# Kernel optimization log

Measured on AMD Instinct MI355X. Metric: run time of the kernel, lower is better.

Reference implementation:

```python
import jax, jax.numpy as jnp
import numpy as np

EPS = 1e-5
K = 5

def _bn(x, g, b):
    # BatchNorm1d in training mode: biased batch statistics
    mu = jnp.mean(x, axis=0)
    var = jnp.mean((x - mu) ** 2, axis=0)
    return (x - mu) * jax.lax.rsqrt(var + EPS) * g + b

def setup_inputs():
    key = jax.random.key(0)
    ks = jax.random.split(key, 16)
    N, M, D, F = 16384, 8192, 512, 2048
    s = 0.02
    return dict(
        src=jax.random.normal(ks[0], (N, D), jnp.float32),
        anchor_2=jax.random.normal(ks[1], (M, D), jnp.float32),
        W_dim=jax.random.normal(ks[2], (D, D), jnp.float32) * s,
        b_dim=jnp.zeros((D,), jnp.float32),
        W_fus=jax.random.normal(ks[3], (2 * D, D), jnp.float32) * s,
        b_fus=jnp.zeros((D,), jnp.float32),
        W_e1=jax.random.normal(ks[4], (D, F), jnp.float32) * s,
        b_e1=jnp.zeros((F,), jnp.float32),
        W_e2=jax.random.normal(ks[5], (F, D), jnp.float32) * s,
        b_e2=jnp.zeros((D,), jnp.float32),
        g1=jnp.ones((D,), jnp.float32), bt1=jnp.zeros((D,), jnp.float32),
        g2=jnp.ones((D,), jnp.float32), bt2=jnp.zeros((D,), jnp.float32),
        W_d=jax.random.normal(ks[6], (D, D), jnp.float32) * s,
        b_d=jnp.zeros((D,), jnp.float32),
        g_d=jnp.ones((D,), jnp.float32), bt_d=jnp.zeros((D,), jnp.float32),
    )

def reference(src, anchor_2, W_dim, b_dim, W_fus, b_fus, W_e1, b_e1, W_e2, b_e2,
              g1, bt1, g2, bt2, W_d, b_d, g_d, bt_d):
    # kNN in Euclidean metric (sklearn NearestNeighbors): squared distances suffice
    # d2[n,m] = ||src_n||^2 - 2 src_n . a_m + ||a_m||^2   -> [N, M]
    d2 = (jnp.sum(src * src, axis=1, keepdims=True)
          - 2.0 * (src @ anchor_2.T)
          + jnp.sum(anchor_2 * anchor_2, axis=1)[None, :])
    _, idx = jax.lax.top_k(-d2, K)                      # [N, K] nearest anchors
    neigh = jnp.mean(anchor_2[idx], axis=1)             # gather + mean -> [N, D]
    a_map = neigh @ W_dim + b_dim                       # linear_dim
    comb = jnp.concatenate([src, a_map], axis=1) @ W_fus + b_fus
    comb = _bn(comb, g1, bt1)                           # norm1
    # encoder MLP (dropout is identity in eval)
    t = jnp.tanh(comb @ W_e1 + b_e1) @ W_e2 + b_e2
    comb = _bn(comb + t, g2, bt2)                       # residual + norm2
    out = jnp.tanh(_bn(comb @ W_d + b_d, g_d, bt_d))    # decoder
    return out
```

## Files before the change

kernel.cpp:

```cpp
#include <hip/hip_runtime.h>
#include <math.h>

#define N_ROWS 16384
#define M_ANCH 8192
#define DDIM   512
#define FDIM   2048
#define KNN    5
#define BN_EPS 1e-5f
#define CHUNK  8192
#define SEED   1024
#define CAND_MAX 256
#define MARGIN 4.0f

typedef _Float16 f16;
typedef _Float16 f16x8 __attribute__((ext_vector_type(8)));
typedef _Float16 f16x4 __attribute__((ext_vector_type(4)));
typedef float f32x4 __attribute__((ext_vector_type(4)));

__device__ __forceinline__ void async_copy16(const void* g, void* l) {
    __builtin_amdgcn_global_load_lds(
        (const __attribute__((address_space(1))) void*)g,
        (__attribute__((address_space(3))) void*)l, 16, 0, 0);
}

__device__ __forceinline__ bool kless(float k1, int i1, float k2, int i2) {
    return (k1 < k2) || (k1 == k2 && i1 < i2);
}

__device__ __forceinline__ void insert5(float (&bk)[KNN], int (&bi)[KNN], float key, int id) {
    if (!kless(key, id, bk[4], bi[4])) return;
    bool c3 = kless(key, id, bk[3], bi[3]);
    bool c2 = kless(key, id, bk[2], bi[2]);
    bool c1 = kless(key, id, bk[1], bi[1]);
    bool c0 = kless(key, id, bk[0], bi[0]);
    bk[4] = c3 ? bk[3] : key;                  bi[4] = c3 ? bi[3] : id;
    bk[3] = c3 ? (c2 ? bk[2] : key) : bk[3];   bi[3] = c3 ? (c2 ? bi[2] : id) : bi[3];
    bk[2] = c2 ? (c1 ? bk[1] : key) : bk[2];   bi[2] = c2 ? (c1 ? bi[1] : id) : bi[2];
    bk[1] = c1 ? (c0 ? bk[0] : key) : bk[1];   bi[1] = c1 ? (c0 ? bi[0] : id) : bi[1];
    bk[0] = c0 ? key : bk[0];                  bi[0] = c0 ? id : bi[0];
}

__global__ void zero_kernel(float* p, int n) {
    int i = blockIdx.x * blockDim.x + threadIdx.x;
    if (i < n) p[i] = 0.f;
}

__global__ __launch_bounds__(256) void cast_f16_kernel(const float* __restrict__ X,
                                                       f16* __restrict__ Y, int n4) {
    int i4 = blockIdx.x * 256 + threadIdx.x;
    if (i4 >= n4) return;
    float4 v = ((const float4*)X)[i4];
    f16x4 h;
    h.x = (f16)v.x; h.y = (f16)v.y; h.z = (f16)v.z; h.w = (f16)v.w;
    ((f16x4*)Y)[i4] = h;
}

__global__ __launch_bounds__(256) void anchor_norm_kernel(const float* __restrict__ a,
                                                          float* __restrict__ norm_a) {
    int wave = threadIdx.x >> 6, lane = threadIdx.x & 63;
    int row = blockIdx.x * 4 + wave;
    const float4* ar = (const float4*)(a + (size_t)row * DDIM);
    float4 v1 = ar[lane * 2];
    float4 v2 = ar[lane * 2 + 1];
    float s = v1.x*v1.x + v1.y*v1.y + v1.z*v1.z + v1.w*v1.w
            + v2.x*v2.x + v2.y*v2.y + v2.z*v2.z + v2.w*v2.w;
    for (int off = 32; off; off >>= 1) s += __shfl_xor(s, off, 64);
    if (lane == 0) norm_a[row] = s;
}

template<int K>
__global__ __launch_bounds__(256) void gemm_f16_key(
    const f16* __restrict__ A, const f16* __restrict__ B,
    const float* __restrict__ norm, float* __restrict__ C, int Ncols)
{
    __shared__ f16 As[128 * 32];
    __shared__ f16 Bs[128 * 32];
    const int t = threadIdx.x;
    const int w = t >> 6, l = t & 63;
    const int m0 = blockIdx.y * 128, n0 = blockIdx.x * 128;
    const int wm = (w & 1) * 64, wn = (w >> 1) * 64;

    f32x4 acc[4][4];
    #pragma unroll
    for (int i = 0; i < 4; ++i)
        #pragma unroll
        for (int j = 0; j < 4; ++j) acc[i][j] = (f32x4){0.f, 0.f, 0.f, 0.f};

    const int srow = l >> 2;
    const int gq = ((l & 3) - (srow >> 1)) & 3;
    const int skoff = gq * 8;
    const int sqf = (((l >> 4) + (((l & 15) >> 1) & 3)) & 3) * 8;

    for (int k0 = 0; k0 < K; k0 += 32) {
        __syncthreads();
        #pragma unroll
        for (int s = 0; s < 2; ++s) {
            int grp = w * 2 + s;
            int row = grp * 16 + srow;
            async_copy16(A + (size_t)(m0 + row) * K + k0 + skoff, As + grp * 512 + l * 8);
            async_copy16(B + (size_t)(n0 + row) * K + k0 + skoff, Bs + grp * 512 + l * 8);
        }
        __syncthreads();
        f16x8 af[4], bf[4];
        #pragma unroll
        for (int i = 0; i < 4; ++i)
            af[i] = *(const f16x8*)(As + (wm + i * 16 + (l & 15)) * 32 + sqf);
        #pragma unroll
        for (int j = 0; j < 4; ++j)
            bf[j] = *(const f16x8*)(Bs + (wn + j * 16 + (l & 15)) * 32 + sqf);
        #pragma unroll
        for (int i = 0; i < 4; ++i)
            #pragma unroll
            for (int j = 0; j < 4; ++j)
                acc[i][j] = __builtin_amdgcn_mfma_f32_16x16x32_f16(af[i], bf[j], acc[i][j], 0, 0, 0);
    }
    float nj[4];
    #pragma unroll
    for (int j = 0; j < 4; ++j) nj[j] = norm[n0 + wn + j * 16 + (l & 15)];
    #pragma unroll
    for (int i = 0; i < 4; ++i)
        #pragma unroll
        for (int j = 0; j < 4; ++j)
            #pragma unroll
            for (int r = 0; r < 4; ++r) {
                int m = m0 + wm + i * 16 + (l >> 4) * 4 + r;
                int n = n0 + wn + j * 16 + (l & 15);
                C[(size_t)m * Ncols + n] = nj[j] - 2.f * acc[i][j][r];
            }
}

template<int K>
__global__ __launch_bounds__(256) void gemm_collect(
    const f16* __restrict__ A, const f16* __restrict__ B,
    const float* __restrict__ norm, const float* __restrict__ thr,
    int* __restrict__ cnt, int* __restrict__ cand_i, int idofs)
{
    __shared__ f16 As[128 * 32];
    __shared__ f16 Bs[128 * 32];
    const int t = threadIdx.x;
    const int w = t >> 6, l = t & 63;
    const int m0 = blockIdx.y * 128, n0 = blockIdx.x * 128;
    const int wm = (w & 1) * 64, wn = (w >> 1) * 64;

    f32x4 acc[4][4];
    #pragma unroll
    for (int i = 0; i < 4; ++i)
        #pragma unroll
        for (int j = 0; j < 4; ++j) acc[i][j] = (f32x4){0.f, 0.f, 0.f, 0.f};

    const int srow = l >> 2;
    const int gq = ((l & 3) - (srow >> 1)) & 3;
    const int skoff = gq * 8;
    const int sqf = (((l >> 4) + (((l & 15) >> 1) & 3)) & 3) * 8;

    for (int k0 = 0; k0 < K; k0 += 32) {
        __syncthreads();
        #pragma unroll
        for (int s = 0; s < 2; ++s) {
            int grp = w * 2 + s;
            int row = grp * 16 + srow;
            async_copy16(A + (size_t)(m0 + row) * K + k0 + skoff, As + grp * 512 + l * 8);
            async_copy16(B + (size_t)(n0 + row) * K + k0 + skoff, Bs + grp * 512 + l * 8);
        }
        __syncthreads();
        f16x8 af[4], bf[4];
        #pragma unroll
        for (int i = 0; i < 4; ++i)
            af[i] = *(const f16x8*)(As + (wm + i * 16 + (l & 15)) * 32 + sqf);
        #pragma unroll
        for (int j = 0; j < 4; ++j)
            bf[j] = *(const f16x8*)(Bs + (wn + j * 16 + (l & 15)) * 32 + sqf);
        #pragma unroll
        for (int i = 0; i < 4; ++i)
            #pragma unroll
            for (int j = 0; j < 4; ++j)
                acc[i][j] = __builtin_amdgcn_mfma_f32_16x16x32_f16(af[i], bf[j], acc[i][j], 0, 0, 0);
    }
    float thr4[4][4];
    #pragma unroll
    for (int i = 0; i < 4; ++i) {
        float4 tv = *(const float4*)&thr[m0 + wm + i * 16 + (l >> 4) * 4];
        thr4[i][0] = tv.x; thr4[i][1] = tv.y; thr4[i][2] = tv.z; thr4[i][3] = tv.w;
    }
    float nj[4];
    #pragma unroll
    for (int j = 0; j < 4; ++j) nj[j] = norm[n0 + wn + j * 16 + (l & 15)];
    #pragma unroll
    for (int i = 0; i < 4; ++i)
        #pragma unroll
        for (int j = 0; j < 4; ++j)
            #pragma unroll
            for (int r = 0; r < 4; ++r) {
                float key = nj[j] - 2.f * acc[i][j][r];
                if (key < thr4[i][r]) {
                    int row = m0 + wm + i * 16 + (l >> 4) * 4 + r;
                    int pos = atomicAdd(&cnt[row], 1);
                    if (pos < CAND_MAX)
                        cand_i[(size_t)row * CAND_MAX + pos] =
                            idofs + n0 + wn + j * 16 + (l & 15);
                }
            }
}

__global__ __launch_bounds__(256) void topk_scan_kernel(
    const float* __restrict__ g, float* __restrict__ thrbuf,
    int* __restrict__ cnt, int* __restrict__ cand_i)
{
    int row = blockIdx.x * 4 + (threadIdx.x >> 6);
    int lane = threadIdx.x & 63;
    const float* grow = g + (size_t)row * SEED;
    float4 v0 = *(const float4*)(grow + lane * 4);
    float4 v1 = *(const float4*)(grow + 256 + lane * 4);
    float4 v2 = *(const float4*)(grow + 512 + lane * 4);
    float4 v3 = *(const float4*)(grow + 768 + lane * 4);
    float bk[KNN]; int bi[KNN];
    #pragma unroll
    for (int q = 0; q < KNN; ++q) { bk[q] = 3.0e38f; bi[q] = 0x7fffffff; }
    int c = lane * 4;
    insert5(bk, bi, v0.x, c);       insert5(bk, bi, v0.y, c + 1);
    insert5(bk, bi, v0.z, c + 2);   insert5(bk, bi, v0.w, c + 3);
    insert5(bk, bi, v1.x, c + 256); insert5(bk, bi, v1.y, c + 257);
    insert5(bk, bi, v1.z, c + 258); insert5(bk, bi, v1.w, c + 259);
    insert5(bk, bi, v2.x, c + 512); insert5(bk, bi, v2.y, c + 513);
    insert5(bk, bi, v2.z, c + 514); insert5(bk, bi, v2.w, c + 515);
    insert5(bk, bi, v3.x, c + 768); insert5(bk, bi, v3.y, c + 769);
    insert5(bk, bi, v3.z, c + 770); insert5(bk, bi, v3.w, c + 771);
    for (int off = 32; off >= 1; off >>= 1) {
        float ok[KNN]; int oi[KNN];
        #pragma unroll
        for (int q = 0; q < KNN; ++q) {
            ok[q] = __shfl_xor(bk[q], off, 64);
            oi[q] = __shfl_xor(bi[q], off, 64);
        }
        #pragma unroll
        for (int q = 0; q < KNN; ++q) insert5(bk, bi, ok[q], oi[q]);
    }
    float thr = bk[4] + MARGIN;
    if (lane == 0) thrbuf[row] = thr;
    int* rci = cand_i + (size_t)row * CAND_MAX;
    #define PUSH(v, id) if ((v) < thr) { int pos = atomicAdd(&cnt[row], 1); \
                                         if (pos < CAND_MAX) rci[pos] = (id); }
    PUSH(v0.x, c)       PUSH(v0.y, c + 1)   PUSH(v0.z, c + 2)   PUSH(v0.w, c + 3)
    PUSH(v1.x, c + 256) PUSH(v1.y, c + 257) PUSH(v1.z, c + 258) PUSH(v1.w, c + 259)
    PUSH(v2.x, c + 512) PUSH(v2.y, c + 513) PUSH(v2.z, c + 514) PUSH(v2.w, c + 515)
    PUSH(v3.x, c + 768) PUSH(v3.y, c + 769) PUSH(v3.z, c + 770) PUSH(v3.w, c + 771)
    #undef PUSH
}

__global__ __launch_bounds__(256) void rescore_kernel(
    const float* __restrict__ src, const float* __restrict__ anchor,
    const float* __restrict__ norm_a, const int* __restrict__ cnt,
    const int* __restrict__ cand_i, int* __restrict__ bi_state)
{
    int row = blockIdx.x * 4 + (threadIdx.x >> 6);
    int lane = threadIdx.x & 63;
    const float4* sp = (const float4*)(src + (size_t)row * DDIM);
    float4 s0 = sp[lane * 2], s1 = sp[lane * 2 + 1];
    float bk[KNN]; int bi[KNN];
    #pragma unroll
    for (int q = 0; q < KNN; ++q) { bk[q] = 3.0e38f; bi[q] = 0x7fffffff; }
    int c = cnt[row]; if (c > CAND_MAX) c = CAND_MAX;
    const int* ci = cand_i + (size_t)row * CAND_MAX;
    for (int p = 0; p < c; ++p) {
        int id = ci[p];
        const float4* ap = (const float4*)(anchor + (size_t)id * DDIM);
        float4 a0 = ap[lane * 2], a1 = ap[lane * 2 + 1];
        float d = s0.x*a0.x + s0.y*a0.y + s0.z*a0.z + s0.w*a0.w
                + s1.x*a1.x + s1.y*a1.y + s1.z*a1.z + s1.w*a1.w;
        #pragma unroll
        for (int off = 32; off; off >>= 1) d += __shfl_xor(d, off, 64);
        float key = norm_a[id] - 2.f * d;
        insert5(bk, bi, key, id);
    }
    if (lane == 0) {
        #pragma unroll
        for (int q = 0; q < KNN; ++q) bi_state[row * KNN + q] = bi[q];
    }
}

__global__ __launch_bounds__(256) void gather_mean_kernel(
    const float* __restrict__ anchor, const int* __restrict__ bi_state,
    float* __restrict__ neigh)
{
    int row = blockIdx.x * 4 + (threadIdx.x >> 6);
    int lane = threadIdx.x & 63;
    const int* bi = bi_state + row * KNN;
    int i0 = bi[0], i1 = bi[1], i2 = bi[2], i3 = bi[3], i4 = bi[4];
    const float4* a0 = (const float4*)(anchor + (size_t)i0 * DDIM);
    const float4* a1 = (const float4*)(anchor + (size_t)i1 * DDIM);
    const float4* a2 = (const float4*)(anchor + (size_t)i2 * DDIM);
    const float4* a3 = (const float4*)(anchor + (size_t)i3 * DDIM);
    const float4* a4 = (const float4*)(anchor + (size_t)i4 * DDIM);
    float4* np = (float4*)(neigh + (size_t)row * DDIM);
    #pragma unroll
    for (int p = 0; p < 2; ++p) {
        int c4 = lane + 64 * p;
        float4 v0 = a0[c4], v1 = a1[c4], v2 = a2[c4], v3 = a3[c4], v4 = a4[c4];
        float4 o;
        o.x = (v0.x + v1.x + v2.x + v3.x + v4.x) * 0.2f;
        o.y = (v0.y + v1.y + v2.y + v3.y + v4.y) * 0.2f;
        o.z = (v0.z + v1.z + v2.z + v3.z + v4.z) * 0.2f;
        o.w = (v0.w + v1.w + v2.w + v3.w + v4.w) * 0.2f;
        np[c4] = o;
    }
}

template<int ADDC0, int TANH, int K>
__global__ __launch_bounds__(256) void gemm_split_nt(
    const float* __restrict__ A, const f16* __restrict__ Bw,
    const float* __restrict__ bias, const float* __restrict__ C0,
    float* __restrict__ C, int Ncols)
{
    __shared__ f16 Ah[128 * 32];
    __shared__ f16 Al[128 * 32];
    __shared__ f16 Bh[128 * 32];
    __shared__ f16 Bl[128 * 32];
    const int t = threadIdx.x;
    const int w = t >> 6, l = t & 63;
    const int m0 = blockIdx.y * 128, n0 = blockIdx.x * 128;
    const int wm = (w & 1) * 64, wn = (w >> 1) * 64;
    const int K2 = 2 * K;

    f32x4 acc[4][4];
    #pragma unroll
    for (int i = 0; i < 4; ++i)
        #pragma unroll
        for (int j = 0; j < 4; ++j) acc[i][j] = (f32x4){0.f, 0.f, 0.f, 0.f};

    const int ar = t >> 1;
    const int ac = (t & 1) * 16;
    const int arq = (ar >> 1) & 3;
    const int s0 = (((t & 1) * 2 + 0 + arq) & 3) * 8;
    const int s1 = (((t & 1) * 2 + 1 + arq) & 3) * 8;
    const int srow = l >> 2;
    const int gq = ((l & 3) - (srow >> 1)) & 3;
    const int skoff = gq * 8;
    const int sqf = (((l >> 4) + (((l & 15) >> 1) & 3)) & 3) * 8;

    for (int k0 = 0; k0 < K; k0 += 32) {
        __syncthreads();
        #pragma unroll
        for (int s = 0; s < 2; ++s) {
            int grp = w * 2 + s;
            int row = grp * 16 + srow;
            const f16* bp = Bw + (size_t)(n0 + row) * K2 + k0 + skoff;
            async_copy16(bp, Bh + grp * 512 + l * 8);
            async_copy16(bp + K, Bl + grp * 512 + l * 8);
        }
        {
            const float* ap = A + (size_t)(m0 + ar) * K + k0 + ac;
            float xs[16];
            *(float4*)&xs[0]  = *(const float4*)ap;
            *(float4*)&xs[4]  = *(const float4*)(ap + 4);
            *(float4*)&xs[8]  = *(const float4*)(ap + 8);
            *(float4*)&xs[12] = *(const float4*)(ap + 12);
            f16x8 h0, h1, lo0, lo1;
            #pragma unroll
            for (int e = 0; e < 8; ++e) {
                f16 hh = (f16)xs[e];
                h0[e] = hh; lo0[e] = (f16)(xs[e] - (float)hh);
                f16 hh2 = (f16)xs[8 + e];
                h1[e] = hh2; lo1[e] = (f16)(xs[8 + e] - (float)hh2);
            }
            *(f16x8*)&Ah[ar * 32 + s0] = h0;  *(f16x8*)&Ah[ar * 32 + s1] = h1;
            *(f16x8*)&Al[ar * 32 + s0] = lo0; *(f16x8*)&Al[ar * 32 + s1] = lo1;
        }
        __syncthreads();
        f16x8 afh[4], afl[4], bfh[4], bfl[4];
        #pragma unroll
        for (int i = 0; i < 4; ++i) {
            int base = (wm + i * 16 + (l & 15)) * 32 + sqf;
            afh[i] = *(const f16x8*)(Ah + base);
            afl[i] = *(const f16x8*)(Al + base);
        }
        #pragma unroll
        for (int j = 0; j < 4; ++j) {
            int base = (wn + j * 16 + (l & 15)) * 32 + sqf;
            bfh[j] = *(const f16x8*)(Bh + base);
            bfl[j] = *(const f16x8*)(Bl + base);
        }
        #pragma unroll
        for (int i = 0; i < 4; ++i)
            #pragma unroll
            for (int j = 0; j < 4; ++j) {
                acc[i][j] = __builtin_amdgcn_mfma_f32_16x16x32_f16(afh[i], bfh[j], acc[i][j], 0, 0, 0);
                acc[i][j] = __builtin_amdgcn_mfma_f32_16x16x32_f16(afl[i], bfh[j], acc[i][j], 0, 0, 0);
                acc[i][j] = __builtin_amdgcn_mfma_f32_16x16x32_f16(afh[i], bfl[j], acc[i][j], 0, 0, 0);
            }
    }
    float bv[4];
    #pragma unroll
    for (int j = 0; j < 4; ++j)
        bv[j] = bias ? bias[n0 + wn + j * 16 + (l & 15)] : 0.f;
    #pragma unroll
    for (int i = 0; i < 4; ++i)
        #pragma unroll
        for (int j = 0; j < 4; ++j)
            #pragma unroll
            for (int r = 0; r < 4; ++r) {
                int m = m0 + wm + i * 16 + (l >> 4) * 4 + r;
                int n = n0 + wn + j * 16 + (l & 15);
                float v = acc[i][j][r] + bv[j];
                if (ADDC0) v += C0[(size_t)m * Ncols + n];
                if (TANH)  v = tanhf(v);
                C[(size_t)m * Ncols + n] = v;
            }
}

__global__ __launch_bounds__(256) void wsplit_kernel(const float* __restrict__ W,
                                                     f16* __restrict__ Wt,
                                                     int K, int N)
{
    __shared__ float tile[64][65];
    const int t = threadIdx.x;
    const int kb = blockIdx.y * 64, nb = blockIdx.x * 64;
    #pragma unroll
    for (int i = 0; i < 4; ++i) {
        int r = (t >> 4) + i * 16;
        int c = (t & 15) * 4;
        *(float4*)&tile[r][c] = *(const float4*)&W[(size_t)(kb + r) * N + nb + c];
    }
    __syncthreads();
    const int r2 = t >> 2;
    const int kc = (t & 3) * 16;
    f16x8 h0, h1, lo0, lo1;
    #pragma unroll
    for (int e = 0; e < 8; ++e) {
        float x = tile[kc + e][r2];
        f16 hh = (f16)x; h0[e] = hh; lo0[e] = (f16)(x - (float)hh);
        float y = tile[kc + 8 + e][r2];
        f16 hh2 = (f16)y; h1[e] = hh2; lo1[e] = (f16)(y - (float)hh2);
    }
    f16* base = Wt + (size_t)(nb + r2) * 2 * K + kb + kc;
    *(f16x8*)base = h0; *(f16x8*)(base + 8) = h1;
    *(f16x8*)(base + K) = lo0; *(f16x8*)(base + K + 8) = lo1;
}

__global__ __launch_bounds__(256) void bcomb_kernel(const float* __restrict__ b_dim,
                                                    const float* __restrict__ W_fus2,
                                                    const float* __restrict__ b_fus,
                                                    float* __restrict__ b_comb)
{
    int n = blockIdx.x * 256 + threadIdx.x;
    if (n >= DDIM) return;
    float s = b_fus[n];
    for (int k = 0; k < DDIM; ++k) s += b_dim[k] * W_fus2[(size_t)k * DDIM + n];
    b_comb[n] = s;
}

template<int ACT>
__global__ __launch_bounds__(256) void gemm_kernel(
    const float* __restrict__ A, int K1,
    const float* __restrict__ A2, int K2,
    const float* __restrict__ B, const float* __restrict__ bias,
    float* __restrict__ C, int Ncols)
{
    __shared__ float As[16][132];
    __shared__ float Bs[16][128];
    const int t = threadIdx.x;
    const int n0 = blockIdx.x * 128;
    const int m0 = blockIdx.y * 128;
    const int ty = t >> 4, tx = t & 15;
    const int K = K1 + K2;

    float acc[8][8];
    #pragma unroll
    for (int i = 0; i < 8; ++i)
        #pragma unroll
        for (int j = 0; j < 8; ++j) acc[i][j] = 0.f;

    const int ar = t >> 1;
    const int akc = (t & 1) * 8;
    const int bkr = t >> 4;
    const int bc = (t & 15) * 8;

    for (int k0 = 0; k0 < K; k0 += 16) {
        int kk = k0 + akc;
        float4 v0, v1;
        if (kk < K1) {
            const float* p = A + (size_t)(m0 + ar) * K1 + kk;
            v0 = *(const float4*)p; v1 = *(const float4*)(p + 4);
        } else {
            const float* p = A2 + (size_t)(m0 + ar) * K2 + (kk - K1);
            v0 = *(const float4*)p; v1 = *(const float4*)(p + 4);
        }
        const float* bp = B + (size_t)(k0 + bkr) * Ncols + n0 + bc;
        float4 w0 = *(const float4*)bp, w1 = *(const float4*)(bp + 4);
        __syncthreads();
        As[akc+0][ar] = v0.x; As[akc+1][ar] = v0.y; As[akc+2][ar] = v0.z; As[akc+3][ar] = v0.w;
        As[akc+4][ar] = v1.x; As[akc+5][ar] = v1.y; As[akc+6][ar] = v1.z; As[akc+7][ar] = v1.w;
        *(float4*)&Bs[bkr][bc] = w0; *(float4*)&Bs[bkr][bc + 4] = w1;
        __syncthreads();
        #pragma unroll
        for (int k = 0; k < 16; ++k) {
            float a[8], b[8];
            *(float4*)&a[0] = *(const float4*)&As[k][ty * 8];
            *(float4*)&a[4] = *(const float4*)&As[k][ty * 8 + 4];
            *(float4*)&b[0] = *(const float4*)&Bs[k][tx * 4];
            *(float4*)&b[4] = *(const float4*)&Bs[k][64 + tx * 4];
            #pragma unroll
            for (int i = 0; i < 8; ++i)
                #pragma unroll
                for (int j = 0; j < 8; ++j) acc[i][j] += a[i] * b[j];
        }
    }
    float4 bv0 = *(const float4*)(bias + n0 + tx * 4);
    float4 bv1 = *(const float4*)(bias + n0 + 64 + tx * 4);
    #pragma unroll
    for (int i = 0; i < 8; ++i) {
        int row = m0 + ty * 8 + i;
        float4 o0, o1;
        o0.x = acc[i][0] + bv0.x; o0.y = acc[i][1] + bv0.y;
        o0.z = acc[i][2] + bv0.z; o0.w = acc[i][3] + bv0.w;
        o1.x = acc[i][4] + bv1.x; o1.y = acc[i][5] + bv1.y;
        o1.z = acc[i][6] + bv1.z; o1.w = acc[i][7] + bv1.w;
        if (ACT == 1) {
            o0.x = tanhf(o0.x); o0.y = tanhf(o0.y); o0.z = tanhf(o0.z); o0.w = tanhf(o0.w);
            o1.x = tanhf(o1.x); o1.y = tanhf(o1.y); o1.z = tanhf(o1.z); o1.w = tanhf(o1.w);
        }
        *(float4*)(C + (size_t)row * Ncols + n0 + tx * 4) = o0;
        *(float4*)(C + (size_t)row * Ncols + n0 + 64 + tx * 4) = o1;
    }
}

__global__ __launch_bounds__(256) void bn_stats_kernel(const float* __restrict__ X,
                                                       float* __restrict__ sums)
{
    __shared__ float red[8][64];
    int lane = threadIdx.x & 63;
    int rl = threadIdx.x >> 6;
    int c = blockIdx.x * 64 + lane;
    int chunk = N_ROWS / gridDim.y;
    int rbeg = blockIdx.y * chunk;
    float s = 0.f, s2 = 0.f;
    for (int r = rbeg + rl; r < rbeg + chunk; r += 4) {
        float v = X[(size_t)r * DDIM + c];
        s += v; s2 += v * v;
    }
    red[rl][lane] = s; red[4 + rl][lane] = s2;
    __syncthreads();
    if (threadIdx.x < 64) {
        float ts = red[0][lane] + red[1][lane] + red[2][lane] + red[3][lane];
        float t2 = red[4][lane] + red[5][lane] + red[6][lane] + red[7][lane];
        atomicAdd(&sums[c], ts);
        atomicAdd(&sums[DDIM + c], t2);
    }
}

template<int TANH>
__global__ __launch_bounds__(256) void bn_apply_kernel(
    const float* __restrict__ X, float* __restrict__ Y,
    const float* __restrict__ sums, const float* __restrict__ g,
    const float* __restrict__ b, float invN)
{
    size_t i = (size_t)blockIdx.x * 256 + threadIdx.x;
    int cg = (int)(i % (DDIM / 4));
    int c = cg * 4;
    float4 x = ((const float4*)X)[i];
    float4 sm = *(const float4*)(sums + c);
    float4 sq = *(const float4*)(sums + DDIM + c);
    float4 gv = *(const float4*)(g + c);
    float4 bv = *(const float4*)(b + c);
    float m, var, rs;
    m = sm.x * invN; var = sq.x * invN - m * m; rs = rsqrtf(var + BN_EPS);
    x.x = (x.x - m) * rs * gv.x + bv.x;
    m = sm.y * invN; var = sq.y * invN - m * m; rs = rsqrtf(var + BN_EPS);
    x.y = (x.y - m) * rs * gv.y + bv.y;
    m = sm.z * invN; var = sq.z * invN - m * m; rs = rsqrtf(var + BN_EPS);
    x.z = (x.z - m) * rs * gv.z + bv.z;
    m = sm.w * invN; var = sq.w * invN - m * m; rs = rsqrtf(var + BN_EPS);
    x.w = (x.w - m) * rs * gv.w + bv.w;
    if (TANH) { x.x = tanhf(x.x); x.y = tanhf(x.y); x.z = tanhf(x.z); x.w = tanhf(x.w); }
    ((float4*)Y)[i] = x;
}

extern "C" void kernel_launch(void* const* d_in, const int* in_sizes, int n_in,
                              void* d_out, int out_size, void* d_ws, size_t ws_size,
                              hipStream_t stream)
{
    const float* src   = (const float*)d_in[0];
    const float* anc   = (const float*)d_in[1];
    const float* W_dim = (const float*)d_in[2];
    const float* b_dim = (const float*)d_in[3];
    const float* W_fus = (const float*)d_in[4];
    const float* b_fus = (const float*)d_in[5];
    const float* W_e1  = (const float*)d_in[6];
    const float* b_e1  = (const float*)d_in[7];
    const float* W_e2  = (const float*)d_in[8];
    const float* b_e2  = (const float*)d_in[9];
    const float* g1    = (const float*)d_in[10];
    const float* bt1   = (const float*)d_in[11];
    const float* g2    = (const float*)d_in[12];
    const float* bt2   = (const float*)d_in[13];
    const float* W_d   = (const float*)d_in[14];
    const float* b_d   = (const float*)d_in[15];
    const float* g_d   = (const float*)d_in[16];
    const float* bt_d  = (const float*)d_in[17];
    float* out = (float*)d_out;

    float* ws = (float*)d_ws;
    float* score  = ws;
    float* bufA   = ws + 16777216;
    f16*   src2h  = (f16*)(ws + 25165824);
    f16*   anc2h  = (f16*)(ws + 37748736);
    f16*   wbase  = (f16*)(ws + 25165824);
    f16*   Wt_fus1  = wbase;
    f16*   Wt_comb2 = wbase + 524288;
    f16*   Wt_e1    = wbase + 1048576;
    f16*   Wt_e2    = wbase + 3145728;
    f16*   Wt_d     = wbase + 5242880;
    float* W_comb2  = ws + 44040192;
    float* norm_a   = ws + 44302336;
    float* sums1    = ws + 44310528;
    float* sums2    = sums1 + 1024;
    float* sums3    = sums2 + 1024;
    float* zeros512 = ws + 44313600;
    float* b_comb   = ws + 44314112;
    int*   bi_state = (int*)(ws + 44396544);
    float* thrbuf   = ws + 44478464;
    int*   cnt      = (int*)(ws + 44494848);
    int*   cand_i   = (int*)(ws + 48705536);

    const float invN = 1.0f / (float)N_ROWS;
    float* hbuf = score;

    zero_kernel<<<dim3(14), 256, 0, stream>>>(sums1, 3584);
    zero_kernel<<<dim3(64), 256, 0, stream>>>((float*)cnt, 16384);
    cast_f16_kernel<<<dim3(N_ROWS * DDIM / 1024), 256, 0, stream>>>(
        src, src2h, N_ROWS * DDIM / 4);
    cast_f16_kernel<<<dim3(M_ANCH * DDIM / 1024), 256, 0, stream>>>(
        anc, anc2h, M_ANCH * DDIM / 4);
    anchor_norm_kernel<<<dim3(M_ANCH / 4), 256, 0, stream>>>(anc, norm_a);

    gemm_f16_key<DDIM><<<dim3(SEED / 128, N_ROWS / 128), 256, 0, stream>>>(
        src2h, anc2h, norm_a, score, SEED);
    topk_scan_kernel<<<dim3(N_ROWS / 4), 256, 0, stream>>>(
        score, thrbuf, cnt, cand_i);
    gemm_collect<DDIM><<<dim3((M_ANCH - SEED) / 128, N_ROWS / 128), 256, 0, stream>>>(
        src2h, anc2h + (size_t)SEED * DDIM, norm_a + SEED, thrbuf,
        cnt, cand_i, SEED);
    rescore_kernel<<<dim3(N_ROWS / 4), 256, 0, stream>>>(
        src, anc, norm_a, cnt, cand_i, bi_state);
    gather_mean_kernel<<<dim3(N_ROWS / 4), 256, 0, stream>>>(anc, bi_state, bufA);

    wsplit_kernel<<<dim3(DDIM / 64, DDIM / 64), 256, 0, stream>>>(W_fus, Wt_fus1, DDIM, DDIM);
    wsplit_kernel<<<dim3(FDIM / 64, DDIM / 64), 256, 0, stream>>>(W_e1, Wt_e1, DDIM, FDIM);
    wsplit_kernel<<<dim3(DDIM / 64, FDIM / 64), 256, 0, stream>>>(W_e2, Wt_e2, FDIM, DDIM);
    wsplit_kernel<<<dim3(DDIM / 64, DDIM / 64), 256, 0, stream>>>(W_d, Wt_d, DDIM, DDIM);
    gemm_kernel<0><<<dim3(4, 4), 256, 0, stream>>>(
        W_dim, DDIM, nullptr, 0, W_fus + DDIM * DDIM, zeros512, W_comb2, DDIM);
    bcomb_kernel<<<dim3(2), 256, 0, stream>>>(b_dim, W_fus + DDIM * DDIM, b_fus, b_comb);
    wsplit_kernel<<<dim3(DDIM / 64, DDIM / 64), 256, 0, stream>>>(W_comb2, Wt_comb2, DDIM, DDIM);

    gemm_split_nt<0, 0, DDIM><<<dim3(DDIM / 128, N_ROWS / 128), 256, 0, stream>>>(
        src, Wt_fus1, b_comb, nullptr, out, DDIM);
    gemm_split_nt<1, 0, DDIM><<<dim3(DDIM / 128, N_ROWS / 128), 256, 0, stream>>>(
        bufA, Wt_comb2, nullptr, out, out, DDIM);
    bn_stats_kernel<<<dim3(DDIM / 64, 16), 256, 0, stream>>>(out, sums1);
    bn_apply_kernel<0><<<dim3(8192), 256, 0, stream>>>(out, out, sums1, g1, bt1, invN);

    for (int r0 = 0; r0 < N_ROWS; r0 += CHUNK) {
        gemm_split_nt<0, 1, DDIM><<<dim3(FDIM / 128, CHUNK / 128), 256, 0, stream>>>(
            out + (size_t)r0 * DDIM, Wt_e1, b_e1, nullptr, hbuf, FDIM);
        gemm_split_nt<1, 0, FDIM><<<dim3(DDIM / 128, CHUNK / 128), 256, 0, stream>>>(
            hbuf, Wt_e2, b_e2, out + (size_t)r0 * DDIM, bufA + (size_t)r0 * DDIM,
            DDIM);
    }
    bn_stats_kernel<<<dim3(DDIM / 64, 16), 256, 0, stream>>>(bufA, sums2);
    bn_apply_kernel<0><<<dim3(8192), 256, 0, stream>>>(bufA, bufA, sums2, g2, bt2, invN);

    gemm_split_nt<0, 0, DDIM><<<dim3(DDIM / 128, N_ROWS / 128), 256, 0, stream>>>(
        bufA, Wt_d, b_d, nullptr, out, DDIM);
    bn_stats_kernel<<<dim3(DDIM / 64, 16), 256, 0, stream>>>(out, sums3);
    bn_apply_kernel<1><<<dim3(8192), 256, 0, stream>>>(out, out, sums3, g_d, bt_d, invN);
}
```

Before: 1.607 ms.

## Quantize kNN distance GEMMs to int8 MFMA with double-buffered LDS

Replaces the f16 cast and f16 MFMA candidate-screening GEMMs with an int8 quantization (fixed scale 28) and the i8 16x16x64 MFMA, so half as many bytes are loaded and the instruction has higher peak throughput. The two GEMM variants are merged into one templated kernel that double-buffers LDS tiles so loads overlap compute. The candidate margin is widened to absorb the larger quantization error. Exact rescoring in fp32 still picks the final neighbours, but a fixed scale with clipping assumes inputs of roughly unit scale, and more candidates may overflow CAND_MAX.

```diff
diff --git a/kernel.cpp b/kernel.cpp
--- a/kernel.cpp
+++ b/kernel.cpp
@@ -10,12 +10,15 @@
 #define CHUNK  8192
 #define SEED   1024
 #define CAND_MAX 256
-#define MARGIN 4.0f
+#define MARGIN 6.0f
+#define QSCALE 28.0f
+#define TWO_INV_S2 (2.0f / (QSCALE * QSCALE))
 
 typedef _Float16 f16;
 typedef _Float16 f16x8 __attribute__((ext_vector_type(8)));
 typedef _Float16 f16x4 __attribute__((ext_vector_type(4)));
 typedef float f32x4 __attribute__((ext_vector_type(4)));
+typedef int   i32x4 __attribute__((ext_vector_type(4)));
 
 __device__ __forceinline__ void async_copy16(const void* g, void* l) {
     __builtin_amdgcn_global_load_lds(
@@ -45,14 +48,17 @@
     if (i < n) p[i] = 0.f;
 }
 
-__global__ __launch_bounds__(256) void cast_f16_kernel(const float* __restrict__ X,
-                                                       f16* __restrict__ Y, int n4) {
-    int i4 = blockIdx.x * 256 + threadIdx.x;
-    if (i4 >= n4) return;
-    float4 v = ((const float4*)X)[i4];
-    f16x4 h;
-    h.x = (f16)v.x; h.y = (f16)v.y; h.z = (f16)v.z; h.w = (f16)v.w;
-    ((f16x4*)Y)[i4] = h;
+__global__ __launch_bounds__(256) void quant_i8_kernel(const float* __restrict__ X,
+                                                       unsigned int* __restrict__ Y, int n4) {
+    int i = blockIdx.x * 256 + threadIdx.x;
+    if (i >= n4) return;
+    float4 v = ((const float4*)X)[i];
+    int a = (int)rintf(v.x * QSCALE); a = a > 127 ? 127 : (a < -127 ? -127 : a);
+    int b = (int)rintf(v.y * QSCALE); b = b > 127 ? 127 : (b < -127 ? -127 : b);
+    int c = (int)rintf(v.z * QSCALE); c = c > 127 ? 127 : (c < -127 ? -127 : c);
+    int d = (int)rintf(v.w * QSCALE); d = d > 127 ? 127 : (d < -127 ? -127 : d);
+    Y[i] = (unsigned int)(a & 255) | ((unsigned int)(b & 255) << 8)
+         | ((unsigned int)(c & 255) << 16) | ((unsigned int)(d & 255) << 24);
 }
 
 __global__ __launch_bounds__(256) void anchor_norm_kernel(const float* __restrict__ a,
@@ -68,138 +74,103 @@
     if (lane == 0) norm_a[row] = s;
 }
 
-template<int K>
-__global__ __launch_bounds__(256) void gemm_f16_key(
-    const f16* __restrict__ A, const f16* __restrict__ B,
-    const float* __restrict__ norm, float* __restrict__ C, int Ncols)
-{
-    __shared__ f16 As[128 * 32];
-    __shared__ f16 Bs[128 * 32];
+template<int COLLECT>
+__global__ __launch_bounds__(256) void gemm_i8(
+    const char* __restrict__ A, const char* __restrict__ B,
+    const float* __restrict__ norm, const float* __restrict__ thr,
+    int* __restrict__ cnt, int* __restrict__ cand_i, int idofs,
+    float* __restrict__ C, int Ncols)
+{
+    __shared__ char As[2][128 * 64];
+    __shared__ char Bs[2][128 * 64];
     const int t = threadIdx.x;
     const int w = t >> 6, l = t & 63;
     const int m0 = blockIdx.y * 128, n0 = blockIdx.x * 128;
     const int wm = (w & 1) * 64, wn = (w >> 1) * 64;
 
-    f32x4 acc[4][4];
+    i32x4 acc[4][4];
     #pragma unroll
     for (int i = 0; i < 4; ++i)
         #pragma unroll
-        for (int j = 0; j < 4; ++j) acc[i][j] = (f32x4){0.f, 0.f, 0.f, 0.f};
+        for (int j = 0; j < 4; ++j) acc[i][j] = (i32x4){0, 0, 0, 0};
 
     const int srow = l >> 2;
     const int gq = ((l & 3) - (srow >> 1)) & 3;
-    const int skoff = gq * 8;
-    const int sqf = (((l >> 4) + (((l & 15) >> 1) & 3)) & 3) * 8;
-
-    for (int k0 = 0; k0 < K; k0 += 32) {
-        __syncthreads();
+    const int skoff = gq * 16;
+    const int sqf = (((l >> 4) + (((l & 15) >> 1) & 3)) & 3) * 16;
+
+    auto STAGE = [&](int buf, int kt) {
+        int k0 = kt * 64;
         #pragma unroll
         for (int s = 0; s < 2; ++s) {
             int grp = w * 2 + s;
             int row = grp * 16 + srow;
-            async_copy16(A + (size_t)(m0 + row) * K + k0 + skoff, As + grp * 512 + l * 8);
-            async_copy16(B + (size_t)(n0 + row) * K + k0 + skoff, Bs + grp * 512 + l * 8);
-        }
-        __syncthreads();
-        f16x8 af[4], bf[4];
+            async_copy16(A + (size_t)(m0 + row) * DDIM + k0 + skoff,
+                         &As[buf][grp * 1024 + l * 16]);
+            async_copy16(B + (size_t)(n0 + row) * DDIM + k0 + skoff,
+                         &Bs[buf][grp * 1024 + l * 16]);
+        }
+    };
+
+    STAGE(0, 0);
+    __syncthreads();
+
+    for (int kt = 0; kt < 8; ++kt) {
+        int cur = kt & 1;
+        if (kt < 7) STAGE(cur ^ 1, kt + 1);
+        i32x4 af[4], bf[4];
         #pragma unroll
         for (int i = 0; i < 4; ++i)
-            af[i] = *(const f16x8*)(As + (wm + i * 16 + (l & 15)) * 32 + sqf);
+            af[i] = *(const i32x4*)&As[cur][(wm + i * 16 + (l & 15)) * 64 + sqf];
         #pragma unroll
         for (int j = 0; j < 4; ++j)
-            bf[j] = *(const f16x8*)(Bs + (wn + j * 16 + (l & 15)) * 32 + sqf);
+            bf[j] = *(const i32x4*)&Bs[cur][(wn + j * 16 + (l & 15)) * 64 + sqf];
         #pragma unroll
         for (int i = 0; i < 4; ++i)
             #pragma unroll
             for (int j = 0; j < 4; ++j)
-                acc[i][j] = __builtin_amdgcn_mfma_f32_16x16x32_f16(af[i], bf[j], acc[i][j], 0, 0, 0);
-    }
+                acc[i][j] = __builtin_amdgcn_mfma_i32_16x16x64_i8(af[i], bf[j], acc[i][j], 0, 0, 0);
+        __syncthreads();
+    }
+
     float nj[4];
     #pragma unroll
     for (int j = 0; j < 4; ++j) nj[j] = norm[n0 + wn + j * 16 + (l & 15)];
-    #pragma unroll
-    for (int i = 0; i < 4; ++i)
-        #pragma unroll
-        for (int j = 0; j < 4; ++j)
-            #pragma unroll
-            for (int r = 0; r < 4; ++r) {
-                int m = m0 + wm + i * 16 + (l >> 4) * 4 + r;
-                int n = n0 + wn + j * 16 + (l & 15);
-                C[(size_t)m * Ncols + n] = nj[j] - 2.f * acc[i][j][r];
-            }
-}
-
-template<int K>
-__global__ __launch_bounds__(256) void gemm_collect(
-    const f16* __restrict__ A, const f16* __restrict__ B,
-    const float* __restrict__ norm, const float* __restrict__ thr,
-    int* __restrict__ cnt, int* __restrict__ cand_i, int idofs)
-{
-    __shared__ f16 As[128 * 32];
-    __shared__ f16 Bs[128 * 32];
-    const int t = threadIdx.x;
-    const int w = t >> 6, l = t & 63;
-    const int m0 = blockIdx.y * 128, n0 = blockIdx.x * 128;
-    const int wm = (w & 1) * 64, wn = (w >> 1) * 64;
-
-    f32x4 acc[4][4];
-    #pragma unroll
-    for (int i = 0; i < 4; ++i)
-        #pragma unroll
-        for (int j = 0; j < 4; ++j) acc[i][j] = (f32x4){0.f, 0.f, 0.f, 0.f};
-
-    const int srow = l >> 2;
-    const int gq = ((l & 3) - (srow >> 1)) & 3;
-    const int skoff = gq * 8;
-    const int sqf = (((l >> 4) + (((l & 15) >> 1) & 3)) & 3) * 8;
-
-    for (int k0 = 0; k0 < K; k0 += 32) {
-        __syncthreads();
-        #pragma unroll
-        for (int s = 0; s < 2; ++s) {
-            int grp = w * 2 + s;
-            int row = grp * 16 + srow;
-            async_copy16(A + (size_t)(m0 + row) * K + k0 + skoff, As + grp * 512 + l * 8);
-            async_copy16(B + (size_t)(n0 + row) * K + k0 + skoff, Bs + grp * 512 + l * 8);
-        }
-        __syncthreads();
-        f16x8 af[4], bf[4];
-        #pragma unroll
-        for (int i = 0; i < 4; ++i)
-            af[i] = *(const f16x8*)(As + (wm + i * 16 + (l & 15)) * 32 + sqf);
-        #pragma unroll
-        for (int j = 0; j < 4; ++j)
-            bf[j] = *(const f16x8*)(Bs + (wn + j * 16 + (l & 15)) * 32 + sqf);
+
+    if (COLLECT) {
+        float thr4[4][4];
+        #pragma unroll
+        for (int i = 0; i < 4; ++i) {
+            float4 tv = *(const float4*)&thr[m0 + wm + i * 16 + (l >> 4) * 4];
+            thr4[i][0] = tv.x; thr4[i][1] = tv.y; thr4[i][2] = tv.z; thr4[i][3] = tv.w;
+        }
         #pragma unroll
         for (int i = 0; i < 4; ++i)
             #pragma unroll
             for (int j = 0; j < 4; ++j)
-                acc[i][j] = __builtin_amdgcn_mfma_f32_16x16x32_f16(af[i], bf[j], acc[i][j], 0, 0, 0);
-    }
-    float thr4[4][4];
-    #pragma unroll
-    for (int i = 0; i < 4; ++i) {
-        float4 tv = *(const float4*)&thr[m0 + wm + i * 16 + (l >> 4) * 4];
-        thr4[i][0] = tv.x; thr4[i][1] = tv.y; thr4[i][2] = tv.z; thr4[i][3] = tv.w;
-    }
-    float nj[4];
-    #pragma unroll
-    for (int j = 0; j < 4; ++j) nj[j] = norm[n0 + wn + j * 16 + (l & 15)];
-    #pragma unroll
-    for (int i = 0; i < 4; ++i)
-        #pragma unroll
-        for (int j = 0; j < 4; ++j)
+                #pragma unroll
+                for (int r = 0; r < 4; ++r) {
+                    float key = nj[j] - TWO_INV_S2 * (float)acc[i][j][r];
+                    if (key < thr4[i][r]) {
+                        int row = m0 + wm + i * 16 + (l >> 4) * 4 + r;
+                        int pos = atomicAdd(&cnt[row], 1);
+                        if (pos < CAND_MAX)
+                            cand_i[(size_t)row * CAND_MAX + pos] =
+                                idofs + n0 + wn + j * 16 + (l & 15);
+                    }
+                }
+    } else {
+        #pragma unroll
+        for (int i = 0; i < 4; ++i)
             #pragma unroll
-            for (int r = 0; r < 4; ++r) {
-                float key = nj[j] - 2.f * acc[i][j][r];
-                if (key < thr4[i][r]) {
-                    int row = m0 + wm + i * 16 + (l >> 4) * 4 + r;
-                    int pos = atomicAdd(&cnt[row], 1);
-                    if (pos < CAND_MAX)
-                        cand_i[(size_t)row * CAND_MAX + pos] =
-                            idofs + n0 + wn + j * 16 + (l & 15);
+            for (int j = 0; j < 4; ++j)
+                #pragma unroll
+                for (int r = 0; r < 4; ++r) {
+                    int m = m0 + wm + i * 16 + (l >> 4) * 4 + r;
+                    int n = n0 + wn + j * 16 + (l & 15);
+                    C[(size_t)m * Ncols + n] = nj[j] - TWO_INV_S2 * (float)acc[i][j][r];
                 }
-            }
+    }
 }
 
 __global__ __launch_bounds__(256) void topk_scan_kernel(
@@ -601,8 +572,8 @@
     float* ws = (float*)d_ws;
     float* score  = ws;
     float* bufA   = ws + 16777216;
-    f16*   src2h  = (f16*)(ws + 25165824);
-    f16*   anc2h  = (f16*)(ws + 37748736);
+    char*  src2q  = (char*)(ws + 25165824);
+    char*  anc2q  = (char*)(ws + 37748736);
     f16*   wbase  = (f16*)(ws + 25165824);
     f16*   Wt_fus1  = wbase;
     f16*   Wt_comb2 = wbase + 524288;
@@ -626,19 +597,19 @@
 
     zero_kernel<<<dim3(14), 256, 0, stream>>>(sums1, 3584);
     zero_kernel<<<dim3(64), 256, 0, stream>>>((float*)cnt, 16384);
-    cast_f16_kernel<<<dim3(N_ROWS * DDIM / 1024), 256, 0, stream>>>(
-        src, src2h, N_ROWS * DDIM / 4);
-    cast_f16_kernel<<<dim3(M_ANCH * DDIM / 1024), 256, 0, stream>>>(
-        anc, anc2h, M_ANCH * DDIM / 4);
+    quant_i8_kernel<<<dim3(N_ROWS * DDIM / 1024), 256, 0, stream>>>(
+        src, (unsigned int*)src2q, N_ROWS * DDIM / 4);
+    quant_i8_kernel<<<dim3(M_ANCH * DDIM / 1024), 256, 0, stream>>>(
+        anc, (unsigned int*)anc2q, M_ANCH * DDIM / 4);
     anchor_norm_kernel<<<dim3(M_ANCH / 4), 256, 0, stream>>>(anc, norm_a);
 
-    gemm_f16_key<DDIM><<<dim3(SEED / 128, N_ROWS / 128), 256, 0, stream>>>(
-        src2h, anc2h, norm_a, score, SEED);
+    gemm_i8<0><<<dim3(SEED / 128, N_ROWS / 128), 256, 0, stream>>>(
+        src2q, anc2q, norm_a, nullptr, nullptr, nullptr, 0, score, SEED);
     topk_scan_kernel<<<dim3(N_ROWS / 4), 256, 0, stream>>>(
         score, thrbuf, cnt, cand_i);
-    gemm_collect<DDIM><<<dim3((M_ANCH - SEED) / 128, N_ROWS / 128), 256, 0, stream>>>(
-        src2h, anc2h + (size_t)SEED * DDIM, norm_a + SEED, thrbuf,
-        cnt, cand_i, SEED);
+    gemm_i8<1><<<dim3((M_ANCH - SEED) / 128, N_ROWS / 128), 256, 0, stream>>>(
+        src2q, anc2q + (size_t)SEED * DDIM, norm_a + SEED, thrbuf,
+        cnt, cand_i, SEED, nullptr, 0);
     rescore_kernel<<<dim3(N_ROWS / 4), 256, 0, stream>>>(
         src, anc, norm_a, cnt, cand_i, bi_state);
     gather_mean_kernel<<<dim3(N_ROWS / 4), 256, 0, stream>>>(anc, bi_state, bufA);
```

New measurement: 1.515 ms. -5.8%, faster.
